# Performance work log

Hardware: AMD Instinct MI355X
Metric: run time of the kernel (lower is better)

Reference implementation:

```python
import math
import jax, jax.numpy as jnp
import numpy as np

IN_D = 16
H_DIM = 256
NB_STEPS = 50
B = 8192


def _cc_weights(nb_steps):
    # Clenshaw-Curtis quadrature weights and nodes, exactly as the torch code.
    k = np.arange(0, nb_steps + 1, dtype=np.float64).reshape(-1, 1)
    lam = np.cos(k @ k.T * math.pi / nb_steps)
    lam[:, 0] = 0.5
    lam[:, -1] = 0.5 * lam[:, -1]
    lam = lam * 2.0 / nb_steps
    W = np.arange(0, nb_steps + 1, dtype=np.float64).reshape(-1, 1)
    W[1::2] = 0.0
    W = 2.0 / (1.0 - W ** 2)
    W[0] = 1.0
    W[1::2] = 0.0
    cc = (lam.T @ W).astype(np.float32)  # [nb_steps+1, 1]
    steps = np.cos(np.arange(0, nb_steps + 1) * math.pi / nb_steps).astype(np.float32)  # [nb_steps+1]
    return jnp.asarray(cc), jnp.asarray(steps)


def setup_inputs() -> dict:
    key = jax.random.key(0)
    ks = jax.random.split(key, 16)
    s = 0.05
    return {
        "x": jax.random.normal(ks[0], (B, 1), jnp.float32),
        "h": jax.random.normal(ks[1], (B, IN_D - 1), jnp.float32),
        "iw1": jax.random.normal(ks[2], (H_DIM, IN_D), jnp.float32) * s,
        "ib1": jax.random.normal(ks[3], (H_DIM,), jnp.float32) * s,
        "iw2": jax.random.normal(ks[4], (H_DIM, H_DIM), jnp.float32) * s,
        "ib2": jax.random.normal(ks[5], (H_DIM,), jnp.float32) * s,
        "iw3": jax.random.normal(ks[6], (1, H_DIM), jnp.float32) * s,
        "ib3": jax.random.normal(ks[7], (1,), jnp.float32) * s,
        "nw1": jax.random.normal(ks[8], (H_DIM, IN_D - 1), jnp.float32) * s,
        "nb1": jax.random.normal(ks[9], (H_DIM,), jnp.float32) * s,
        "nw2": jax.random.normal(ks[10], (H_DIM, H_DIM), jnp.float32) * s,
        "nb2": jax.random.normal(ks[11], (H_DIM,), jnp.float32) * s,
        "nw3": jax.random.normal(ks[12], (2, H_DIM), jnp.float32) * s,
        "nb3": jax.random.normal(ks[13], (2,), jnp.float32) * s,
        "nb_steps": NB_STEPS,
    }


def _integrand(z, iw1, ib1, iw2, ib2, iw3, ib3):
    # IntegrandNN: Linear-ReLU-Linear-ReLU-Linear-ELU, then +1.0
    a = jax.nn.relu(z @ iw1.T + ib1)
    a = jax.nn.relu(a @ iw2.T + ib2)
    return jax.nn.elu(a @ iw3.T + ib3) + 1.0


def reference(x, h, iw1, ib1, iw2, ib2, iw3, ib3, nw1, nb1, nw2, nb2, nw3, nb3, nb_steps):
    cc, steps = _cc_weights(int(nb_steps))  # cc: [N+1,1], steps: [N+1]
    Bn, n_pts = x.shape[0], int(nb_steps) + 1
    # x0 = 0, so quadrature nodes X_k = x * (steps_k + 1) / 2 -> [B, N+1, 1]
    X = x[:, None, :] * ((steps[None, :, None] + 1.0) * 0.5)
    Xf = X.reshape(-1, 1)                                             # [B*(N+1), 1]
    Hf = jnp.broadcast_to(h[:, None, :], (Bn, n_pts, h.shape[1])).reshape(-1, h.shape[1])
    z = jnp.concatenate([Xf, Hf], axis=1)                             # [B*(N+1), in_d]
    f = _integrand(z, iw1, ib1, iw2, ib2, iw3, ib3).reshape(Bn, n_pts, 1)
    integral = jnp.sum(f * cc[None, :, :], axis=1) * x * 0.5          # [B, 1]
    # conditioner net on h: Linear-ReLU-Linear-ReLU-Linear -> [B, 2]
    a = jax.nn.relu(h @ nw1.T + nb1)
    a = jax.nn.relu(a @ nw2.T + nb2)
    out = a @ nw3.T + nb3
    offset = out[:, :1]
    scaling = jnp.exp(out[:, 1:2])
    return scaling * integral + offset
```

## Files before the change

kernel.cpp:

```cpp
#include <hip/hip_runtime.h>
#include <hip/hip_bf16.h>
#include <math.h>

#define BATCH 8192
#define HD    256
#define NPTS  51
#define MTOT  (BATCH*NPTS)

typedef __bf16 bf16x8 __attribute__((ext_vector_type(8)));
typedef float  f32x4  __attribute__((ext_vector_type(4)));

#define OFF_IW2P  0
#define OFF_NW2B  131072
#define OFF_W1X   262144
#define OFF_CC    263168
#define OFF_STEPS 263424
#define OFF_OFFS  263680
#define OFF_SCAL  296448
#define OFF_G1    329216
#define OFF_A1N   8717824
#define OFF_FV0   OFF_A1N
#define OFF_FV1   (OFF_A1N + 1671168)

__device__ __forceinline__ unsigned short f2bf(float f) {
    union { float f; unsigned u; } v; v.f = f;
    unsigned r = v.u + 0x7FFFu + ((v.u >> 16) & 1u);
    return (unsigned short)(r >> 16);
}

__device__ __forceinline__ unsigned pk2bf(float lo, float hi) {
    __hip_bfloat162 t = __float22bfloat162_rn(float2{lo, hi});
    union { __hip_bfloat162 b; unsigned u; } v; v.b = t;
    return v.u;
}

__global__ void k01_prep(const float* __restrict__ iw2, const float* __restrict__ nw2,
                         const float* __restrict__ nw1, const float* __restrict__ iw1,
                         const float* __restrict__ ib1, const float* __restrict__ nb1,
                         const float* __restrict__ h,
                         unsigned short* iw2p, unsigned short* nw2b, float* w1xs,
                         float* cc, float* steps,
                         float* __restrict__ g1, unsigned short* __restrict__ a1n) {
    int blk = blockIdx.x, tid = threadIdx.x;
    if (blk < 256) {
        int t = blk * 256 + tid;
        int n = t >> 8, k = t & 255;
        int half = n >> 7, nl = n & 127, c = k >> 3, j = k & 7;
        iw2p[half * 32768 + c * 1024 + nl * 8 + j] = f2bf(iw2[t]);
        nw2b[t] = f2bf(nw2[t]);
    } else if (blk < 768) {
        __shared__ float hs[16][15];
        int b0 = (blk - 256) * 16, n = tid;
        if (tid < 240) { int bb = tid / 15, j = tid % 15; hs[bb][j] = h[(b0 + bb) * 15 + j]; }
        __syncthreads();
        float ir[16], nr[15];
        const float4* ip = (const float4*)(iw1 + n * 16);
        ((float4*)ir)[0] = ip[0]; ((float4*)ir)[1] = ip[1];
        ((float4*)ir)[2] = ip[2]; ((float4*)ir)[3] = ip[3];
        #pragma unroll
        for (int j = 0; j < 15; ++j) nr[j] = nw1[n * 15 + j];
        float bi = ib1[n], bn = nb1[n];
        #pragma unroll
        for (int bb = 0; bb < 16; ++bb) {
            float g = bi, a = bn;
            #pragma unroll
            for (int j = 0; j < 15; ++j) { float hv = hs[bb][j]; g += hv * ir[j + 1]; a += hv * nr[j]; }
            int b = b0 + bb;
            g1[b * 256 + n]  = g;
            a1n[b * 256 + n] = f2bf(fmaxf(a, 0.f));
        }
    } else {
        w1xs[tid] = iw1[tid * 16];
        const double PI_D = 3.14159265358979323846264338327950288;
        if (tid <= 50) {
            int j = tid;
            double s = 0.0;
            for (int i = 0; i <= 50; i += 2) {
                double w = (i == 0) ? 1.0 : 2.0 / (1.0 - (double)(i * i));
                double l;
                if (j == 0)       l = 0.5;
                else if (j == 50) l = 0.5;
                else              l = cos((double)i * (double)j * PI_D / 50.0);
                s += l * w;
            }
            cc[j]    = (float)(s * 2.0 / 50.0);
            steps[j] = (float)cos((double)j * PI_D / 50.0);
        }
    }
}

__launch_bounds__(256, 3)
__global__ void k2_main(const float* __restrict__ x, const float* __restrict__ g1,
                        const float* __restrict__ w1xs, const unsigned short* __restrict__ iw2p,
                        const float* __restrict__ ib2, const float* __restrict__ iw3,
                        const float* __restrict__ steps,
                        float* __restrict__ fv0, float* __restrict__ fv1) {
    __shared__ __align__(16) unsigned char smem[32768];
    float* Pp = (float*)smem;

    int tid = threadIdx.x;
    int bid = blockIdx.x;
    int hf  = bid & 1;
    int m0  = (bid >> 1) * 128;
    int lane = tid & 63, w = tid >> 6;
    int l16 = lane & 15, quad = lane >> 4;

    const unsigned char* bsrc = (const unsigned char*)iw2p + hf * 65536 + tid * 16;

    #pragma unroll
    for (int it = 0; it < 4; ++it)
        __builtin_amdgcn_global_load_lds(
            (const __attribute__((address_space(1))) unsigned int*)(bsrc + it * 4096),
            (__attribute__((address_space(3))) unsigned int*)(smem + tid * 16 + it * 4096),
            16, 0, 0);

    float xs_[2]; int gb_[2];
    #pragma unroll
    for (int mt = 0; mt < 2; ++mt) {
        int m = m0 + w * 32 + mt * 16 + l16;
        unsigned b = (unsigned)(((unsigned long long)(unsigned)m * 657931ull) >> 25);
        int p = m - (int)b * 51;
        xs_[mt] = x[b] * (steps[p] + 1.f) * 0.5f;
        gb_[mt] = (int)b * 256;
    }

    f32x4 acc[2][8];
    #pragma unroll
    for (int mt = 0; mt < 2; ++mt)
        #pragma unroll
        for (int nt = 0; nt < 8; ++nt)
            acc[mt][nt] = (f32x4){0.f, 0.f, 0.f, 0.f};

    #pragma unroll
    for (int kc = 0; kc < 4; ++kc) {
        __syncthreads();
        if (kc < 3) {
            const unsigned char* s2 = bsrc + (kc + 1) * 16384;
            unsigned char* d2 = smem + ((kc + 1) & 1) * 16384 + tid * 16;
            #pragma unroll
            for (int it = 0; it < 4; ++it)
                __builtin_amdgcn_global_load_lds(
                    (const __attribute__((address_space(1))) unsigned int*)(s2 + it * 4096),
                    (__attribute__((address_space(3))) unsigned int*)(d2 + it * 4096),
                    16, 0, 0);
        }
        const unsigned short* Bl = (const unsigned short*)(smem + (kc & 1) * 16384);
        #pragma unroll
        for (int s = 0; s < 2; ++s) {
            int ks = kc * 2 + s;
            int ko = ks * 32 + quad * 8;
            int cl = s * 4 + quad;
            bf16x8 bfr[8];
            #pragma unroll
            for (int nt = 0; nt < 8; ++nt)
                bfr[nt] = *(const bf16x8*)(Bl + (cl * 128 + nt * 16 + l16) * 8);
            float4 w0 = ((const float4*)(w1xs + ko))[0];
            float4 w1 = ((const float4*)(w1xs + ko))[1];
            #pragma unroll
            for (int mt = 0; mt < 2; ++mt) {
                const float* gp = g1 + gb_[mt] + ko;
                float4 ga  = ((const float4*)gp)[0];
                float4 gb2 = ((const float4*)gp)[1];
                float xs = xs_[mt];
                float a0 = fmaxf(ga.x  + xs * w0.x, 0.f);
                float a1 = fmaxf(ga.y  + xs * w0.y, 0.f);
                float a2 = fmaxf(ga.z  + xs * w0.z, 0.f);
                float a3 = fmaxf(ga.w  + xs * w0.w, 0.f);
                float a4 = fmaxf(gb2.x + xs * w1.x, 0.f);
                float a5 = fmaxf(gb2.y + xs * w1.y, 0.f);
                float a6 = fmaxf(gb2.z + xs * w1.z, 0.f);
                float a7 = fmaxf(gb2.w + xs * w1.w, 0.f);
                union { uint4 u; bf16x8 v; } af;
                af.u.x = pk2bf(a0, a1); af.u.y = pk2bf(a2, a3);
                af.u.z = pk2bf(a4, a5); af.u.w = pk2bf(a6, a7);
                #pragma unroll
                for (int nt = 0; nt < 8; ++nt)
                    acc[mt][nt] = __builtin_amdgcn_mfma_f32_16x16x32_bf16(af.v, bfr[nt], acc[mt][nt], 0, 0, 0);
            }
        }
    }

    float pf[2][4];
    #pragma unroll
    for (int mt = 0; mt < 2; ++mt)
        #pragma unroll
        for (int i = 0; i < 4; ++i) pf[mt][i] = 0.f;
    #pragma unroll
    for (int nt = 0; nt < 8; ++nt) {
        int n = hf * 128 + nt * 16 + l16;
        float bias = ib2[n], w3 = iw3[n];
        #pragma unroll
        for (int mt = 0; mt < 2; ++mt)
            #pragma unroll
            for (int i = 0; i < 4; ++i) {
                float v = acc[mt][nt][i] + bias;
                v = v > 0.f ? v : 0.f;
                pf[mt][i] += v * w3;
            }
    }
    __syncthreads();
    #pragma unroll
    for (int mt = 0; mt < 2; ++mt)
        #pragma unroll
        for (int i = 0; i < 4; ++i) {
            int row = w * 32 + mt * 16 + quad * 4 + i;
            Pp[row * 20 + l16] = pf[mt][i];
        }
    __syncthreads();
    if (tid < 128) {
        const float4* pp = (const float4*)(Pp + tid * 20);
        float4 v0 = pp[0], v1 = pp[1], v2 = pp[2], v3 = pp[3];
        float s = v0.x + v0.y + v0.z + v0.w + v1.x + v1.y + v1.z + v1.w
                + v2.x + v2.y + v2.z + v2.w + v3.x + v3.y + v3.z + v3.w;
        (hf ? fv1 : fv0)[m0 + tid] = s;
    }
}

__launch_bounds__(256, 4)
__global__ void k3_nnet(const unsigned short* __restrict__ a1n, const unsigned short* __restrict__ nw2b,
                        const float* __restrict__ nb2, const float* __restrict__ nw3,
                        const float* __restrict__ nb3, float* __restrict__ offs,
                        float* __restrict__ scal) {
    __shared__ float Pp[4 * 2 * 16];
    int tid = threadIdx.x;
    int m0 = blockIdx.x * 16;
    int lane = tid & 63, w = tid >> 6, l16 = lane & 15, quad = lane >> 4;

    f32x4 acc[4];
    #pragma unroll
    for (int nt = 0; nt < 4; ++nt)
        acc[nt] = (f32x4){0.f, 0.f, 0.f, 0.f};

    #pragma unroll
    for (int ks = 0; ks < 8; ++ks) {
        bf16x8 af, bfr[4];
        af = *(const bf16x8*)(a1n + (m0 + l16) * 256 + ks * 32 + quad * 8);
        #pragma unroll
        for (int nt = 0; nt < 4; ++nt)
            bfr[nt] = *(const bf16x8*)(nw2b + (w * 64 + nt * 16 + l16) * 256 + ks * 32 + quad * 8);
        #pragma unroll
        for (int nt = 0; nt < 4; ++nt)
            acc[nt] = __builtin_amdgcn_mfma_f32_16x16x32_bf16(af, bfr[nt], acc[nt], 0, 0, 0);
    }

    float p0[4], p1[4];
    #pragma unroll
    for (int i = 0; i < 4; ++i) { p0[i] = 0.f; p1[i] = 0.f; }
    #pragma unroll
    for (int nt = 0; nt < 4; ++nt) {
        int n = w * 64 + nt * 16 + l16;
        float bias = nb2[n], wa = nw3[n], wb = nw3[256 + n];
        #pragma unroll
        for (int i = 0; i < 4; ++i) {
            float v = acc[nt][i] + bias;
            v = v > 0.f ? v : 0.f;
            p0[i] += v * wa;
            p1[i] += v * wb;
        }
    }
    #pragma unroll
    for (int mask = 1; mask < 16; mask <<= 1)
        #pragma unroll
        for (int i = 0; i < 4; ++i) {
            p0[i] += __shfl_xor(p0[i], mask, 64);
            p1[i] += __shfl_xor(p1[i], mask, 64);
        }
    if (l16 == 0) {
        #pragma unroll
        for (int i = 0; i < 4; ++i) {
            int r = quad * 4 + i;
            Pp[w * 32 + r]      = p0[i];
            Pp[w * 32 + 16 + r] = p1[i];
        }
    }
    __syncthreads();
    if (tid < 16) {
        float s0 = Pp[tid]      + Pp[32 + tid] + Pp[64 + tid] + Pp[96 + tid]  + nb3[0];
        float s1 = Pp[16 + tid] + Pp[48 + tid] + Pp[80 + tid] + Pp[112 + tid] + nb3[1];
        offs[m0 + tid] = s0;
        scal[m0 + tid] = __expf(s1);
    }
}

__global__ void k4_final(const float* __restrict__ x, const float* __restrict__ fv0,
                         const float* __restrict__ fv1, const float* __restrict__ ib3,
                         const float* __restrict__ cc,
                         const float* __restrict__ offs, const float* __restrict__ scal,
                         float* __restrict__ out) {
    int tid = threadIdx.x;
    int wv = tid >> 6, lane = tid & 63;
    int b = blockIdx.x * 4 + wv;
    float v = 0.f;
    if (lane < 51) {
        int m = b * 51 + lane;
        float s = fv0[m] + fv1[m] + ib3[0];
        float f = s > 0.f ? s + 1.f : __expf(s);
        v = f * cc[lane];
    }
    #pragma unroll
    for (int mask = 1; mask < 64; mask <<= 1) v += __shfl_xor(v, mask, 64);
    if (lane == 0)
        out[b] = scal[b] * (0.5f * x[b] * v) + offs[b];
}

extern "C" void kernel_launch(void* const* d_in, const int* in_sizes, int n_in,
                              void* d_out, int out_size, void* d_ws, size_t ws_size,
                              hipStream_t stream) {
    const float* x   = (const float*)d_in[0];
    const float* h   = (const float*)d_in[1];
    const float* iw1 = (const float*)d_in[2];
    const float* ib1 = (const float*)d_in[3];
    const float* iw2 = (const float*)d_in[4];
    const float* ib2 = (const float*)d_in[5];
    const float* iw3 = (const float*)d_in[6];
    const float* ib3 = (const float*)d_in[7];
    const float* nw1 = (const float*)d_in[8];
    const float* nb1 = (const float*)d_in[9];
    const float* nw2 = (const float*)d_in[10];
    const float* nb2 = (const float*)d_in[11];
    const float* nw3 = (const float*)d_in[12];
    const float* nb3 = (const float*)d_in[13];
    float* out = (float*)d_out;

    char* ws = (char*)d_ws;
    unsigned short* iw2p = (unsigned short*)(ws + OFF_IW2P);
    unsigned short* nw2b = (unsigned short*)(ws + OFF_NW2B);
    float* w1xs  = (float*)(ws + OFF_W1X);
    float* cc    = (float*)(ws + OFF_CC);
    float* steps = (float*)(ws + OFF_STEPS);
    float* offs  = (float*)(ws + OFF_OFFS);
    float* scal  = (float*)(ws + OFF_SCAL);
    float* g1    = (float*)(ws + OFF_G1);
    unsigned short* a1n = (unsigned short*)(ws + OFF_A1N);
    float* fv0   = (float*)(ws + OFF_FV0);
    float* fv1   = (float*)(ws + OFF_FV1);

    k01_prep<<<dim3(769), dim3(256), 0, stream>>>(iw2, nw2, nw1, iw1, ib1, nb1, h,
                                                  iw2p, nw2b, w1xs, cc, steps, g1, a1n);
    k3_nnet<<<dim3(BATCH / 16), dim3(256), 0, stream>>>(a1n, nw2b, nb2, nw3, nb3, offs, scal);
    k2_main<<<dim3((MTOT / 128) * 2), dim3(256), 0, stream>>>(x, g1, w1xs, iw2p, ib2, iw3,
                                                              steps, fv0, fv1);
    k4_final<<<dim3(BATCH / 4), dim3(256), 0, stream>>>(x, fv0, fv1, ib3, cc, offs, scal, out);
}
```

Before: 196.9 us.

## Fuse conditioner net into prep kernel and double k2 row tile

```diff
diff --git a/kernel.cpp b/kernel.cpp
--- a/kernel.cpp
+++ b/kernel.cpp
@@ -11,16 +11,14 @@
 typedef float  f32x4  __attribute__((ext_vector_type(4)));
 
 #define OFF_IW2P  0
-#define OFF_NW2B  131072
-#define OFF_W1X   262144
-#define OFF_CC    263168
-#define OFF_STEPS 263424
-#define OFF_OFFS  263680
-#define OFF_SCAL  296448
-#define OFF_G1    329216
-#define OFF_A1N   8717824
-#define OFF_FV0   OFF_A1N
-#define OFF_FV1   (OFF_A1N + 1671168)
+#define OFF_W1X   131072
+#define OFF_CC    132096
+#define OFF_STEPS 132352
+#define OFF_OFFS  132608
+#define OFF_SCAL  165376
+#define OFF_G1    198144
+#define OFF_FV0   8586752
+#define OFF_FV1   10257920
 
 __device__ __forceinline__ unsigned short f2bf(float f) {
     union { float f; unsigned u; } v; v.f = f;
@@ -34,23 +32,41 @@
     return v.u;
 }
 
-__global__ void k01_prep(const float* __restrict__ iw2, const float* __restrict__ nw2,
-                         const float* __restrict__ nw1, const float* __restrict__ iw1,
-                         const float* __restrict__ ib1, const float* __restrict__ nb1,
-                         const float* __restrict__ h,
-                         unsigned short* iw2p, unsigned short* nw2b, float* w1xs,
-                         float* cc, float* steps,
-                         float* __restrict__ g1, unsigned short* __restrict__ a1n) {
+__global__ void k1_fused(const float* __restrict__ iw2, const float* __restrict__ nw1,
+                         const float* __restrict__ iw1, const float* __restrict__ ib1,
+                         const float* __restrict__ nb1, const float* __restrict__ h,
+                         const float* __restrict__ nw2, const float* __restrict__ nb2,
+                         const float* __restrict__ nw3, const float* __restrict__ nb3,
+                         unsigned short* iw2p, float* w1xs, float* cc, float* steps,
+                         float* __restrict__ g1, float* __restrict__ offs,
+                         float* __restrict__ scal) {
     int blk = blockIdx.x, tid = threadIdx.x;
     if (blk < 256) {
         int t = blk * 256 + tid;
         int n = t >> 8, k = t & 255;
         int half = n >> 7, nl = n & 127, c = k >> 3, j = k & 7;
         iw2p[half * 32768 + c * 1024 + nl * 8 + j] = f2bf(iw2[t]);
-        nw2b[t] = f2bf(nw2[t]);
-    } else if (blk < 768) {
+    } else if (blk == 256) {
+        w1xs[tid] = iw1[tid * 16];
+        const float PI_F = 3.14159265358979323846f;
+        if (tid <= 50) {
+            int j = tid;
+            float s = 0.f;
+            for (int i = 0; i <= 50; i += 2) {
+                float w = (i == 0) ? 1.f : 2.f / (1.f - (float)(i * i));
+                float l;
+                if (j == 0 || j == 50) l = 0.5f;
+                else { int r = (i * j) % 100; l = __cosf((float)r * (PI_F / 50.f)); }
+                s += l * w;
+            }
+            cc[j]    = s * (2.f / 50.f);
+            steps[j] = __cosf((float)j * (PI_F / 50.f));
+        }
+    } else {
         __shared__ float hs[16][15];
-        int b0 = (blk - 256) * 16, n = tid;
+        __shared__ unsigned short a1s[16][264];
+        __shared__ float Pp[4 * 2 * 16];
+        int b0 = (blk - 257) * 16, n = tid;
         if (tid < 240) { int bb = tid / 15, j = tid % 15; hs[bb][j] = h[(b0 + bb) * 15 + j]; }
         __syncthreads();
         float ir[16], nr[15];
@@ -65,26 +81,65 @@
             float g = bi, a = bn;
             #pragma unroll
             for (int j = 0; j < 15; ++j) { float hv = hs[bb][j]; g += hv * ir[j + 1]; a += hv * nr[j]; }
-            int b = b0 + bb;
-            g1[b * 256 + n]  = g;
-            a1n[b * 256 + n] = f2bf(fmaxf(a, 0.f));
-        }
-    } else {
-        w1xs[tid] = iw1[tid * 16];
-        const double PI_D = 3.14159265358979323846264338327950288;
-        if (tid <= 50) {
-            int j = tid;
-            double s = 0.0;
-            for (int i = 0; i <= 50; i += 2) {
-                double w = (i == 0) ? 1.0 : 2.0 / (1.0 - (double)(i * i));
-                double l;
-                if (j == 0)       l = 0.5;
-                else if (j == 50) l = 0.5;
-                else              l = cos((double)i * (double)j * PI_D / 50.0);
-                s += l * w;
-            }
-            cc[j]    = (float)(s * 2.0 / 50.0);
-            steps[j] = (float)cos((double)j * PI_D / 50.0);
+            g1[(b0 + bb) * 256 + n] = g;
+            a1s[bb][n] = f2bf(fmaxf(a, 0.f));
+        }
+        __syncthreads();
+
+        int lane = tid & 63, w = tid >> 6, l16 = lane & 15, quad = lane >> 4;
+        f32x4 acc[4];
+        #pragma unroll
+        for (int nt = 0; nt < 4; ++nt) acc[nt] = (f32x4){0.f, 0.f, 0.f, 0.f};
+        #pragma unroll
+        for (int ks = 0; ks < 8; ++ks) {
+            bf16x8 af = *(const bf16x8*)&a1s[l16][ks * 32 + quad * 8];
+            #pragma unroll
+            for (int nt = 0; nt < 4; ++nt) {
+                const float* np = nw2 + (w * 64 + nt * 16 + l16) * 256 + ks * 32 + quad * 8;
+                float4 f0 = ((const float4*)np)[0];
+                float4 f1 = ((const float4*)np)[1];
+                union { uint4 u; bf16x8 v; } bf;
+                bf.u.x = pk2bf(f0.x, f0.y); bf.u.y = pk2bf(f0.z, f0.w);
+                bf.u.z = pk2bf(f1.x, f1.y); bf.u.w = pk2bf(f1.z, f1.w);
+                acc[nt] = __builtin_amdgcn_mfma_f32_16x16x32_bf16(af, bf.v, acc[nt], 0, 0, 0);
+            }
+        }
+        float p0[4], p1[4];
+        #pragma unroll
+        for (int i = 0; i < 4; ++i) { p0[i] = 0.f; p1[i] = 0.f; }
+        #pragma unroll
+        for (int nt = 0; nt < 4; ++nt) {
+            int nn = w * 64 + nt * 16 + l16;
+            float bias = nb2[nn], wa = nw3[nn], wb = nw3[256 + nn];
+            #pragma unroll
+            for (int i = 0; i < 4; ++i) {
+                float v = acc[nt][i] + bias;
+                v = v > 0.f ? v : 0.f;
+                p0[i] += v * wa;
+                p1[i] += v * wb;
+            }
+        }
+        #pragma unroll
+        for (int mask = 1; mask < 16; mask <<= 1)
+            #pragma unroll
+            for (int i = 0; i < 4; ++i) {
+                p0[i] += __shfl_xor(p0[i], mask, 64);
+                p1[i] += __shfl_xor(p1[i], mask, 64);
+            }
+        if (l16 == 0) {
+            #pragma unroll
+            for (int i = 0; i < 4; ++i) {
+                int r = quad * 4 + i;
+                Pp[w * 32 + r]      = p0[i];
+                Pp[w * 32 + 16 + r] = p1[i];
+            }
+        }
+        __syncthreads();
+        if (tid < 16) {
+            float s0 = Pp[tid]      + Pp[32 + tid] + Pp[64 + tid] + Pp[96 + tid]  + nb3[0];
+            float s1 = Pp[16 + tid] + Pp[48 + tid] + Pp[80 + tid] + Pp[112 + tid] + nb3[1];
+            offs[b0 + tid] = s0;
+            scal[b0 + tid] = __expf(s1);
         }
     }
 }
@@ -101,7 +156,7 @@
     int tid = threadIdx.x;
     int bid = blockIdx.x;
     int hf  = bid & 1;
-    int m0  = (bid >> 1) * 128;
+    int m0  = (bid >> 1) * 256;
     int lane = tid & 63, w = tid >> 6;
     int l16 = lane & 15, quad = lane >> 4;
 
@@ -114,19 +169,19 @@
             (__attribute__((address_space(3))) unsigned int*)(smem + tid * 16 + it * 4096),
             16, 0, 0);
 
-    float xs_[2]; int gb_[2];
-    #pragma unroll
-    for (int mt = 0; mt < 2; ++mt) {
-        int m = m0 + w * 32 + mt * 16 + l16;
+    float xs_[4]; int gb_[4];
+    #pragma unroll
+    for (int mt = 0; mt < 4; ++mt) {
+        int m = m0 + w * 64 + mt * 16 + l16;
         unsigned b = (unsigned)(((unsigned long long)(unsigned)m * 657931ull) >> 25);
         int p = m - (int)b * 51;
         xs_[mt] = x[b] * (steps[p] + 1.f) * 0.5f;
         gb_[mt] = (int)b * 256;
     }
 
-    f32x4 acc[2][8];
-    #pragma unroll
-    for (int mt = 0; mt < 2; ++mt)
+    f32x4 acc[4][8];
+    #pragma unroll
+    for (int mt = 0; mt < 4; ++mt)
         #pragma unroll
         for (int nt = 0; nt < 8; ++nt)
             acc[mt][nt] = (f32x4){0.f, 0.f, 0.f, 0.f};
@@ -157,7 +212,7 @@
             float4 w0 = ((const float4*)(w1xs + ko))[0];
             float4 w1 = ((const float4*)(w1xs + ko))[1];
             #pragma unroll
-            for (int mt = 0; mt < 2; ++mt) {
+            for (int mt = 0; mt < 4; ++mt) {
                 const float* gp = g1 + gb_[mt] + ko;
                 float4 ga  = ((const float4*)gp)[0];
                 float4 gb2 = ((const float4*)gp)[1];
@@ -180,9 +235,9 @@
         }
     }
 
-    float pf[2][4];
-    #pragma unroll
-    for (int mt = 0; mt < 2; ++mt)
+    float pf[4][4];
+    #pragma unroll
+    for (int mt = 0; mt < 4; ++mt)
         #pragma unroll
         for (int i = 0; i < 4; ++i) pf[mt][i] = 0.f;
     #pragma unroll
@@ -190,7 +245,7 @@
         int n = hf * 128 + nt * 16 + l16;
         float bias = ib2[n], w3 = iw3[n];
         #pragma unroll
-        for (int mt = 0; mt < 2; ++mt)
+        for (int mt = 0; mt < 4; ++mt)
             #pragma unroll
             for (int i = 0; i < 4; ++i) {
                 float v = acc[mt][nt][i] + bias;
@@ -200,85 +255,19 @@
     }
     __syncthreads();
     #pragma unroll
-    for (int mt = 0; mt < 2; ++mt)
+    for (int mt = 0; mt < 4; ++mt)
         #pragma unroll
         for (int i = 0; i < 4; ++i) {
-            int row = w * 32 + mt * 16 + quad * 4 + i;
+            int row = w * 64 + mt * 16 + quad * 4 + i;
             Pp[row * 20 + l16] = pf[mt][i];
         }
     __syncthreads();
-    if (tid < 128) {
+    {
         const float4* pp = (const float4*)(Pp + tid * 20);
         float4 v0 = pp[0], v1 = pp[1], v2 = pp[2], v3 = pp[3];
         float s = v0.x + v0.y + v0.z + v0.w + v1.x + v1.y + v1.z + v1.w
                 + v2.x + v2.y + v2.z + v2.w + v3.x + v3.y + v3.z + v3.w;
         (hf ? fv1 : fv0)[m0 + tid] = s;
-    }
-}
-
-__launch_bounds__(256, 4)
-__global__ void k3_nnet(const unsigned short* __restrict__ a1n, const unsigned short* __restrict__ nw2b,
-                        const float* __restrict__ nb2, const float* __restrict__ nw3,
-                        const float* __restrict__ nb3, float* __restrict__ offs,
-                        float* __restrict__ scal) {
-    __shared__ float Pp[4 * 2 * 16];
-    int tid = threadIdx.x;
-    int m0 = blockIdx.x * 16;
-    int lane = tid & 63, w = tid >> 6, l16 = lane & 15, quad = lane >> 4;
-
-    f32x4 acc[4];
-    #pragma unroll
-    for (int nt = 0; nt < 4; ++nt)
-        acc[nt] = (f32x4){0.f, 0.f, 0.f, 0.f};
-
-    #pragma unroll
-    for (int ks = 0; ks < 8; ++ks) {
-        bf16x8 af, bfr[4];
-        af = *(const bf16x8*)(a1n + (m0 + l16) * 256 + ks * 32 + quad * 8);
-        #pragma unroll
-        for (int nt = 0; nt < 4; ++nt)
-            bfr[nt] = *(const bf16x8*)(nw2b + (w * 64 + nt * 16 + l16) * 256 + ks * 32 + quad * 8);
-        #pragma unroll
-        for (int nt = 0; nt < 4; ++nt)
-            acc[nt] = __builtin_amdgcn_mfma_f32_16x16x32_bf16(af, bfr[nt], acc[nt], 0, 0, 0);
-    }
-
-    float p0[4], p1[4];
-    #pragma unroll
-    for (int i = 0; i < 4; ++i) { p0[i] = 0.f; p1[i] = 0.f; }
-    #pragma unroll
-    for (int nt = 0; nt < 4; ++nt) {
-        int n = w * 64 + nt * 16 + l16;
-        float bias = nb2[n], wa = nw3[n], wb = nw3[256 + n];
-        #pragma unroll
-        for (int i = 0; i < 4; ++i) {
-            float v = acc[nt][i] + bias;
-            v = v > 0.f ? v : 0.f;
-            p0[i] += v * wa;
-            p1[i] += v * wb;
-        }
-    }
-    #pragma unroll
-    for (int mask = 1; mask < 16; mask <<= 1)
-        #pragma unroll
-        for (int i = 0; i < 4; ++i) {
-            p0[i] += __shfl_xor(p0[i], mask, 64);
-            p1[i] += __shfl_xor(p1[i], mask, 64);
-        }
-    if (l16 == 0) {
-        #pragma unroll
-        for (int i = 0; i < 4; ++i) {
-            int r = quad * 4 + i;
-            Pp[w * 32 + r]      = p0[i];
-            Pp[w * 32 + 16 + r] = p1[i];
-        }
-    }
-    __syncthreads();
-    if (tid < 16) {
-        float s0 = Pp[tid]      + Pp[32 + tid] + Pp[64 + tid] + Pp[96 + tid]  + nb3[0];
-        float s1 = Pp[16 + tid] + Pp[48 + tid] + Pp[80 + tid] + Pp[112 + tid] + nb3[1];
-        offs[m0 + tid] = s0;
-        scal[m0 + tid] = __expf(s1);
     }
 }
 
@@ -324,21 +313,19 @@
 
     char* ws = (char*)d_ws;
     unsigned short* iw2p = (unsigned short*)(ws + OFF_IW2P);
-    unsigned short* nw2b = (unsigned short*)(ws + OFF_NW2B);
     float* w1xs  = (float*)(ws + OFF_W1X);
     float* cc    = (float*)(ws + OFF_CC);
     float* steps = (float*)(ws + OFF_STEPS);
     float* offs  = (float*)(ws + OFF_OFFS);
     float* scal  = (float*)(ws + OFF_SCAL);
     float* g1    = (float*)(ws + OFF_G1);
-    unsigned short* a1n = (unsigned short*)(ws + OFF_A1N);
     float* fv0   = (float*)(ws + OFF_FV0);
     float* fv1   = (float*)(ws + OFF_FV1);
 
-    k01_prep<<<dim3(769), dim3(256), 0, stream>>>(iw2, nw2, nw1, iw1, ib1, nb1, h,
-                                                  iw2p, nw2b, w1xs, cc, steps, g1, a1n);
-    k3_nnet<<<dim3(BATCH / 16), dim3(256), 0, stream>>>(a1n, nw2b, nb2, nw3, nb3, offs, scal);
-    k2_main<<<dim3((MTOT / 128) * 2), dim3(256), 0, stream>>>(x, g1, w1xs, iw2p, ib2, iw3,
+    k1_fused<<<dim3(769), dim3(256), 0, stream>>>(iw2, nw1, iw1, ib1, nb1, h,
+                                                  nw2, nb2, nw3, nb3,
+                                                  iw2p, w1xs, cc, steps, g1, offs, scal);
+    k2_main<<<dim3((MTOT / 256) * 2), dim3(256), 0, stream>>>(x, g1, w1xs, iw2p, ib2, iw3,
                                                               steps, fv0, fv1);
     k4_final<<<dim3(BATCH / 4), dim3(256), 0, stream>>>(x, fv0, fv1, ib3, cc, offs, scal, out);
 }
```

New measurement: 442.8 us. 2.25x slower.
